# Optimization experiments

Hardware: AMD Instinct MI355X
Metric: run time of the kernel (lower is better)

Reference implementation:

```python
import jax, jax.numpy as jnp
import numpy as np

NUM_HEADS = 12
DIM_HEAD = 64
HIDDEN = 768


def _get_rel_pos(size, rel_pos):
    # q_size == k_size: relative coords in [0, 2*size-2]
    idx = jnp.arange(size)[:, None] - jnp.arange(size)[None, :] + (size - 1)
    return rel_pos[idx]  # (size, size, dim_head)


def setup_inputs() -> dict:
    key = jax.random.key(0)
    ks = jax.random.split(key, 5)
    B, H, W, C = 4, 32, 32, HIDDEN
    x = jax.random.normal(ks[0], (B, H, W, C), dtype=jnp.float32)
    w_qkv = jax.random.normal(ks[1], (C, 3 * NUM_HEADS * DIM_HEAD), dtype=jnp.float32) * (C ** -0.5)
    w_out = jax.random.normal(ks[2], (NUM_HEADS * DIM_HEAD, C), dtype=jnp.float32) * ((NUM_HEADS * DIM_HEAD) ** -0.5)
    b_out = jnp.zeros((C,), dtype=jnp.float32)
    rel_pos_h = jax.random.normal(ks[3], (2 * H - 1, DIM_HEAD), dtype=jnp.float32) * 0.02
    rel_pos_w = jax.random.normal(ks[4], (2 * W - 1, DIM_HEAD), dtype=jnp.float32) * 0.02
    return {"x": x, "w_qkv": w_qkv, "w_out": w_out, "b_out": b_out,
            "rel_pos_h": rel_pos_h, "rel_pos_w": rel_pos_w}


def reference(x, w_qkv, w_out, b_out, rel_pos_h, rel_pos_w):
    B, H, W, C = x.shape
    N = H * W
    nh, dh = NUM_HEADS, DIM_HEAD
    # qkv projection: (B, N, 3*nh*dh) split as (qkv, head, dim)
    qkv = x.reshape(B, N, C) @ w_qkv
    qkv = qkv.reshape(B, N, 3, nh, dh).transpose(2, 0, 3, 1, 4)  # (3, B, nh, N, dh)
    q, k, v = qkv[0], qkv[1], qkv[2]
    scale = dh ** -0.5
    attn = jnp.einsum('bhnd,bhmd->bhnm', q, k) * scale  # (B, nh, N, N)
    # decomposed relative positional bias (heads folded into batch)
    Rh = _get_rel_pos(H, rel_pos_h)  # (H, H, dh)
    Rw = _get_rel_pos(W, rel_pos_w)  # (W, W, dh)
    r_q = q.reshape(B * nh, H, W, dh)
    rel_h = jnp.einsum('bhwc,hkc->bhwk', r_q, Rh)  # (B*nh, H, W, H)
    rel_w = jnp.einsum('bhwc,wkc->bhwk', r_q, Rw)  # (B*nh, H, W, W)
    attn = (attn.reshape(B * nh, H, W, H, W)
            + rel_h[:, :, :, :, None]
            + rel_w[:, :, :, None, :]).reshape(B, nh, N, N)
    attn = jax.nn.softmax(attn, axis=-1)
    out = jnp.einsum('bhnm,bhmd->bhnd', attn, v)  # (B, nh, N, dh)
    out = out.transpose(0, 2, 1, 3).reshape(B, N, nh * dh)
    return out @ w_out + b_out  # (B, N, hidden)
```

## Files before the change

kernel.cpp:

```cpp
#include <hip/hip_runtime.h>
#include <cstdint>

#define DEV __device__ __forceinline__

typedef __bf16  bf16x8 __attribute__((ext_vector_type(8)));
typedef short   s16x8  __attribute__((ext_vector_type(8)));
typedef float   f32x4  __attribute__((ext_vector_type(4)));

#define QSCALE 0.18033688011112042f
#define MOFF   17.312340490667560f

DEV unsigned short f2bf(float f){
  union { float f; unsigned u; } v; v.f = f;
  unsigned r = v.u + 0x7fffu + ((v.u >> 16) & 1u);
  return (unsigned short)(r >> 16);
}

DEV unsigned pk2(float lo, float hi){
  unsigned a = __builtin_bit_cast(unsigned, lo) + 0x8000u;
  unsigned b = __builtin_bit_cast(unsigned, hi) + 0x8000u;
  return __builtin_amdgcn_perm(b, a, 0x07060302);
}

DEV void gl2lds16(const void* g, void* l){
  __builtin_amdgcn_global_load_lds((__attribute__((address_space(1))) void*)(void*)(g),
                                   (__attribute__((address_space(3))) void*)(l), 16, 0, 0);
}

DEV f32x4 mfma16(bf16x8 a, bf16x8 b, f32x4 c){
  return __builtin_amdgcn_mfma_f32_16x16x32_bf16(a, b, c, 0, 0, 0);
}

__global__ __launch_bounds__(256) void prep_kernel(const float* __restrict__ x,
                                                   short* __restrict__ xb,
                                                   const float* __restrict__ rph,
                                                   const float* __restrict__ rpw,
                                                   short* __restrict__ rphb,
                                                   short* __restrict__ rpwb,
                                                   const float* __restrict__ w_qkv,
                                                   short* __restrict__ wqT,
                                                   const float* __restrict__ w_out,
                                                   short* __restrict__ woT){
  __shared__ float tb[32][33];
  int b = blockIdx.x;
  if (b < 1536){
    int i = b * 256 + threadIdx.x;
    const float4* in4 = (const float4*)x;
    float4 f0 = in4[i*2], f1 = in4[i*2+1];
    s16x8 o;
    o[0]=(short)f2bf(f0.x); o[1]=(short)f2bf(f0.y); o[2]=(short)f2bf(f0.z); o[3]=(short)f2bf(f0.w);
    o[4]=(short)f2bf(f1.x); o[5]=(short)f2bf(f1.y); o[6]=(short)f2bf(f1.z); o[7]=(short)f2bf(f1.w);
    *(s16x8*)(xb + i*8) = o;
  } else if (b == 1536){
    int t = threadIdx.x;
    for (int j = 0; j < 16; j++){
      int idx = t*16 + j;
      if (idx < 4032){
        rphb[idx] = (short)f2bf(rph[idx] * 8.f);
        rpwb[idx] = (short)f2bf(rpw[idx] * 8.f);
      }
    }
  } else {
    const float* in; short* out; int R, C, bx, by;
    if (b < 3265){ int t = b - 1537; in = w_qkv; out = wqT; R = 768; C = 2304; bx = t % 72; by = t / 72; }
    else         { int t = b - 3265; in = w_out; out = woT; R = 768; C = 768;  bx = t % 24; by = t / 24; }
    int tx = threadIdx.x & 31, ty = threadIdx.x >> 5;
    int c0 = bx * 32, r0 = by * 32;
    for (int i = 0; i < 4; i++)
      tb[ty + i*8][tx] = in[(r0 + ty + i*8)*C + c0 + tx];
    __syncthreads();
    for (int i = 0; i < 4; i++)
      out[(c0 + ty + i*8)*R + r0 + tx] = (short)f2bf(tb[tx][ty + i*8]);
  }
}

__global__ __launch_bounds__(256) void qkv_gemm_kernel(const short* __restrict__ xb,
                                                       const short* __restrict__ wqT,
                                                       short* __restrict__ qb,
                                                       short* __restrict__ kb,
                                                       short* __restrict__ vb){
  __shared__ __align__(16) short As[128*64];
  __shared__ __align__(16) short Bs[96*64];
  const int tid = threadIdx.x, lane = tid & 63, wv = tid >> 6;
  const int quad = lane >> 4, mi = lane & 15;
  const int m0 = blockIdx.x * 128, n0 = blockIdx.y * 96;
  const int wrow = wv >> 1, wcol = wv & 1;
  const int srow = lane >> 3, scs = lane & 7;
  const int sc = scs ^ (srow & 7);
  f32x4 acc[4][3] = {};
  for (int k0 = 0; k0 < 768; k0 += 64){
    __syncthreads();
    for (int i = 0; i < 4; i++){
      int rbase = i*32 + wv*8;
      int row = rbase + srow;
      gl2lds16(xb + (m0+row)*768 + k0 + sc*8, As + rbase*64 + lane*8);
    }
    for (int i = 0; i < 3; i++){
      int rbase = i*32 + wv*8;
      int row = rbase + srow;
      gl2lds16(wqT + (n0+row)*768 + k0 + sc*8, Bs + rbase*64 + lane*8);
    }
    __syncthreads();
    bf16x8 a[2][4], b[2][3];
#pragma unroll
    for (int kk = 0; kk < 2; kk++){
      int ccs = ((quad + kk*4) ^ (mi & 7)) * 8;
      for (int mt = 0; mt < 4; mt++) a[kk][mt] = *(const bf16x8*)(As + (wrow*64 + mt*16 + mi)*64 + ccs);
      for (int nt = 0; nt < 3; nt++) b[kk][nt] = *(const bf16x8*)(Bs + (wcol*48 + nt*16 + mi)*64 + ccs);
    }
#pragma unroll
    for (int kk = 0; kk < 2; kk++)
      for (int mt = 0; mt < 4; mt++)
        for (int nt = 0; nt < 3; nt++)
          acc[mt][nt] = mfma16(a[kk][mt], b[kk][nt], acc[mt][nt]);
  }
  const int which = n0 / 768;
  const float qs = (which == 0) ? QSCALE : 1.0f;
  for (int nt = 0; nt < 3; nt++){
    int j = n0 + wcol*48 + nt*16 + mi;
    int rem = j % 768;
    int head = rem >> 6, d = rem & 63;
    short* dst = (which == 0) ? qb : (which == 1) ? kb : vb;
    for (int mt = 0; mt < 4; mt++)
      for (int r = 0; r < 4; r++){
        int m = m0 + wrow*64 + mt*16 + quad*4 + r;
        int bh = (m >> 10)*12 + head;
        dst[((bh << 10) + (m & 1023))*64 + d] = (short)f2bf(acc[mt][nt][r] * qs);
      }
  }
}

__global__ __launch_bounds__(256) void relvt_kernel(const short* __restrict__ qb,
                                                    const short* __restrict__ rphb,
                                                    const short* __restrict__ rpwb,
                                                    float* __restrict__ relHT,
                                                    float* __restrict__ relW,
                                                    const short* __restrict__ vb,
                                                    short* __restrict__ vtb){
  __shared__ __align__(16) short T[64*64];
  if (blockIdx.x < 1536){
    int wv = threadIdx.x >> 6, lane = threadIdx.x & 63;
    int bid = blockIdx.x*4 + wv;
    int quad = lane >> 4, mi = lane & 15;
    f32x4 acc[2] = {};
    if (bid < 3072){
      int bh = bid >> 6, rest = bid & 63, h = rest >> 1, half = rest & 1;
      const short* qr = qb + (bh*1024 + h*32 + half*16 + mi)*64;
      bf16x8 a0 = *(const bf16x8*)(qr + quad*8);
      bf16x8 a1 = *(const bf16x8*)(qr + 32 + quad*8);
      for (int nt = 0; nt < 2; nt++){
        int kh = nt*16 + mi;
        const short* rr = rphb + (h - kh + 31)*64;
        bf16x8 b0 = *(const bf16x8*)(rr + quad*8);
        bf16x8 b1 = *(const bf16x8*)(rr + 32 + quad*8);
        acc[nt] = mfma16(a0, b0, acc[nt]);
        acc[nt] = mfma16(a1, b1, acc[nt]);
      }
      for (int nt = 0; nt < 2; nt++){
        f32x4 o;
        for (int r = 0; r < 4; r++) o[r] = acc[nt][r] - MOFF;
        *(f32x4*)&relHT[bh*32768 + (nt*16 + mi)*1024 + h*32 + half*16 + quad*4] = o;
      }
    } else {
      int bid2 = bid - 3072, w = bid2 / 96, rt = bid2 % 96;
      int rg = rt*16 + mi, bh = rg >> 5, h = rg & 31;
      const short* qr = qb + (bh*1024 + h*32 + w)*64;
      bf16x8 a0 = *(const bf16x8*)(qr + quad*8);
      bf16x8 a1 = *(const bf16x8*)(qr + 32 + quad*8);
      for (int nt = 0; nt < 2; nt++){
        int kw = nt*16 + mi;
        const short* rr = rpwb + (w - kw + 31)*64;
        bf16x8 b0 = *(const bf16x8*)(rr + quad*8);
        bf16x8 b1 = *(const bf16x8*)(rr + 32 + quad*8);
        acc[nt] = mfma16(a0, b0, acc[nt]);
        acc[nt] = mfma16(a1, b1, acc[nt]);
      }
      for (int nt = 0; nt < 2; nt++)
        for (int r = 0; r < 4; r++){
          int rowg = rt*16 + quad*4 + r;
          relW[(rowg*32 + w)*32 + nt*16 + mi] = acc[nt][r];
        }
    }
  } else {
    int blk = blockIdx.x - 1536;
    int t = threadIdx.x;
    int bh = blk >> 4, t0 = (blk & 15) * 64;
    const short* src = vb + (bh*1024 + t0)*64;
    for (int p = 0; p < 2; p++){
      int row = p*32 + (t >> 3);
      int c = (t & 7) ^ (row & 7);
      gl2lds16(src + row*64 + c*8, T + p*2048 + t*8);
    }
    __syncthreads();
    int d = t >> 2, k4 = t & 3;
    short vals[16];
    for (int j = 0; j < 16; j++){
      int k = k4 + j*4;
      int cs = (d >> 3) ^ (k & 7);
      vals[j] = T[k*64 + cs*8 + (d & 7)];
    }
    short* dst = vtb + (bh*64 + d)*1024 + t0;
    for (int j = 0; j < 16; j++)
      dst[k4 + j*4] = vals[j];
  }
}

__global__ __launch_bounds__(256, 3) void flash_kernel(const short* __restrict__ qb,
                                                       const short* __restrict__ kb,
                                                       const short* __restrict__ vtb,
                                                       const float* __restrict__ relHT,
                                                       const float* __restrict__ relW,
                                                       short* __restrict__ ao){
  __shared__ __align__(16) short Qt[64*64];
  __shared__ __align__(16) short Kt[64*64];
  __shared__ __align__(16) short Vt[64*64];
  __shared__ __align__(16) short Pt[64*64];
  __shared__ __align__(16) float rHs[32*64];
  __shared__ __align__(16) float rWs[64*32];
  const int tid = threadIdx.x, lane = tid & 63, wv = tid >> 6;
  const int quad = lane >> 4, mi = lane & 15;
  const int bh = blockIdx.y, n0 = blockIdx.x * 64;
  const int sw0 = (quad ^ (mi & 7)) * 8;
  const int sw1 = ((quad + 4) ^ (mi & 7)) * 8;
  const int qrow = wv*16 + mi;
  const int srow = lane >> 3;

  const short* kg = kb  + bh*1024*64;
  const short* vg = vtb + bh*64*1024;

  {
    const short* qg  = qb    + (bh*1024 + n0)*64;
    const float* rhg = relHT + bh*32768 + n0;
    const float* rwg = relW  + (bh*1024 + n0)*32;
    for (int i = 0; i < 2; i++){
      int slab = wv*2 + i, rbase = slab*8;
      int row = rbase + srow;
      int c = (lane & 7) ^ (row & 7);
      gl2lds16(qg + row*64 + c*8, Qt + rbase*64 + lane*8);
      int khrow = i*16 + wv*4 + (lane >> 4);
      gl2lds16(rhg + khrow*1024 + (lane & 15)*4, rHs + i*1024 + wv*256 + lane*4);
      gl2lds16(rwg + slab*256 + lane*4, rWs + slab*256 + lane*4);
    }
  }
  __syncthreads();

  bf16x8 qf0 = *(const bf16x8*)(Qt + qrow*64 + sw0);
  bf16x8 qf1 = *(const bf16x8*)(Qt + qrow*64 + sw1);
  float rw[2][4];
#pragma unroll
  for (int s = 0; s < 2; s++)
    for (int r = 0; r < 4; r++)
      rw[s][r] = rWs[qrow*32 + s*16 + quad*4 + r];

  f32x4 O[4] = {};
  float l_ = 0.f;

  for (int step = 0; step < 16; step++){
    {
      const short* kt = kg + step*64*64;
      for (int i = 0; i < 2; i++){
        int slab = wv*2 + i, rbase = slab*8;
        int row = rbase + srow;
        int c = (lane & 7) ^ (row & 7);
        gl2lds16(kt + row*64 + c*8, Kt + rbase*64 + lane*8);
        gl2lds16(vg + row*1024 + step*64 + c*8, Vt + rbase*64 + lane*8);
      }
    }
    __syncthreads();

    f32x4 S[4];
#pragma unroll
    for (int nt = 0; nt < 4; nt++){
      bf16x8 kf0 = *(const bf16x8*)(Kt + (nt*16 + mi)*64 + sw0);
      bf16x8 kf1 = *(const bf16x8*)(Kt + (nt*16 + mi)*64 + sw1);
      f32x4 c = {};
      c = mfma16(kf0, qf0, c);
      c = mfma16(kf1, qf1, c);
      S[nt] = c;
    }
    float kh0 = rHs[(2*step)*64 + qrow];
    float kh1 = rHs[(2*step + 1)*64 + qrow];
#pragma unroll
    for (int nt = 0; nt < 4; nt++){
      float kh = (nt & 2) ? kh1 : kh0;
      for (int r = 0; r < 4; r++){
        float p = __builtin_amdgcn_exp2f(S[nt][r] + kh + rw[nt & 1][r]);
        S[nt][r] = p;
        l_ += p;
      }
    }
#pragma unroll
    for (int nt = 0; nt < 4; nt++){
      unsigned u0 = pk2(S[nt][0], S[nt][1]);
      unsigned u1 = pk2(S[nt][2], S[nt][3]);
      int chunk = (2*nt + (quad >> 1)) ^ (mi & 7);
      uint2 uu; uu.x = u0; uu.y = u1;
      *(uint2*)(Pt + qrow*64 + chunk*8 + (quad & 1)*4) = uu;
    }
    bf16x8 p0 = *(const bf16x8*)(Pt + qrow*64 + sw0);
    bf16x8 p1 = *(const bf16x8*)(Pt + qrow*64 + sw1);
#pragma unroll
    for (int t = 0; t < 4; t++){
      bf16x8 v0 = *(const bf16x8*)(Vt + (t*16 + mi)*64 + sw0);
      bf16x8 v1 = *(const bf16x8*)(Vt + (t*16 + mi)*64 + sw1);
      O[t] = mfma16(p0, v0, O[t]);
      O[t] = mfma16(p1, v1, O[t]);
    }
    __syncthreads();
  }

  l_ += __shfl_xor(l_, 16, 64);
  l_ += __shfl_xor(l_, 32, 64);
  float inv[4];
#pragma unroll
  for (int r = 0; r < 4; r++) inv[r] = 1.f / __shfl(l_, quad*4 + r, 64);
  int b_ = bh / 12, head = bh % 12;
#pragma unroll
  for (int t = 0; t < 4; t++)
    for (int r = 0; r < 4; r++){
      int n = n0 + wv*16 + quad*4 + r;
      ao[(b_*1024 + n)*768 + head*64 + t*16 + mi] = (short)f2bf(O[t][r] * inv[r]);
    }
}

__global__ __launch_bounds__(256) void proj_kernel(const short* __restrict__ ao,
                                                   const short* __restrict__ woT,
                                                   const float* __restrict__ bias,
                                                   float* __restrict__ out){
  __shared__ __align__(16) short As[64*64];
  __shared__ __align__(16) short Bs[96*64];
  const int tid = threadIdx.x, lane = tid & 63, wv = tid >> 6;
  const int quad = lane >> 4, mi = lane & 15;
  const int m0 = blockIdx.x * 64, n0 = blockIdx.y * 96;
  const int wrow = wv >> 1, wcol = wv & 1;
  const int srow = lane >> 3, sc = (lane & 7) ^ (srow & 7);
  f32x4 acc[2][3] = {};
  for (int k0 = 0; k0 < 768; k0 += 64){
    __syncthreads();
    for (int i = 0; i < 2; i++){
      int rbase = i*32 + wv*8, row = rbase + srow;
      gl2lds16(ao + (m0+row)*768 + k0 + sc*8, As + rbase*64 + lane*8);
    }
    for (int i = 0; i < 3; i++){
      int rbase = i*32 + wv*8, row = rbase + srow;
      gl2lds16(woT + (n0+row)*768 + k0 + sc*8, Bs + rbase*64 + lane*8);
    }
    __syncthreads();
    bf16x8 a[2][2], b[2][3];
#pragma unroll
    for (int kk = 0; kk < 2; kk++){
      int ccs = ((quad + kk*4) ^ (mi & 7)) * 8;
      for (int mt = 0; mt < 2; mt++) a[kk][mt] = *(const bf16x8*)(As + (wrow*32 + mt*16 + mi)*64 + ccs);
      for (int nt = 0; nt < 3; nt++) b[kk][nt] = *(const bf16x8*)(Bs + (wcol*48 + nt*16 + mi)*64 + ccs);
    }
#pragma unroll
    for (int kk = 0; kk < 2; kk++)
      for (int mt = 0; mt < 2; mt++)
        for (int nt = 0; nt < 3; nt++)
          acc[mt][nt] = mfma16(a[kk][mt], b[kk][nt], acc[mt][nt]);
  }
  for (int nt = 0; nt < 3; nt++){
    int j = n0 + wcol*48 + nt*16 + mi;
    float bj = bias[j];
    for (int mt = 0; mt < 2; mt++)
      for (int r = 0; r < 4; r++){
        int m = m0 + wrow*32 + mt*16 + quad*4 + r;
        out[m*768 + j] = acc[mt][nt][r] + bj;
      }
  }
}

extern "C" void kernel_launch(void* const* d_in, const int* in_sizes, int n_in,
                              void* d_out, int out_size, void* d_ws, size_t ws_size,
                              hipStream_t stream){
  const float* x     = (const float*)d_in[0];
  const float* w_qkv = (const float*)d_in[1];
  const float* w_out = (const float*)d_in[2];
  const float* b_out = (const float*)d_in[3];
  const float* rph   = (const float*)d_in[4];
  const float* rpw   = (const float*)d_in[5];
  float* out = (float*)d_out;
  char* ws = (char*)d_ws;
  short* xb    = (short*)(ws + 0);
  short* wqT   = (short*)(ws + 6291456);
  short* woT   = (short*)(ws + 9830400);
  short* qb    = (short*)(ws + 11010048);
  short* kb    = (short*)(ws + 17301504);
  short* vb    = (short*)(ws + 23592960);
  short* vtb   = (short*)(ws + 29884416);
  float* relHT = (float*)(ws + 36175872);
  float* relW  = (float*)(ws + 42467328);
  short* rphb  = (short*)(ws + 48758784);
  short* rpwb  = (short*)(ws + 48775168);
  short* ao    = xb;

  prep_kernel<<<3841, 256, 0, stream>>>(x, xb, rph, rpw, rphb, rpwb, w_qkv, wqT, w_out, woT);
  qkv_gemm_kernel<<<dim3(32, 24), 256, 0, stream>>>(xb, wqT, qb, kb, vb);
  relvt_kernel<<<2304, 256, 0, stream>>>(qb, rphb, rpwb, relHT, relW, vb, vtb);
  flash_kernel<<<dim3(16, 48), 256, 0, stream>>>(qb, kb, vtb, relHT, relW, ao);
  proj_kernel<<<dim3(64, 8), 256, 0, stream>>>(ao, woT, b_out, out);
}
```

Measured before the change: 155.9 us.

## Fuse V transpose into QKV GEMM and compute rel_h bias inside flash kernel

After: 153.8 us. About the same (-1.4%).

```diff
diff --git a/kernel.cpp b/kernel.cpp
--- a/kernel.cpp
+++ b/kernel.cpp
@@ -78,7 +78,7 @@
                                                        const short* __restrict__ wqT,
                                                        short* __restrict__ qb,
                                                        short* __restrict__ kb,
-                                                       short* __restrict__ vb){
+                                                       short* __restrict__ vtb){
   __shared__ __align__(16) short As[128*64];
   __shared__ __align__(16) short Bs[96*64];
   const int tid = threadIdx.x, lane = tid & 63, wv = tid >> 6;
@@ -115,101 +115,67 @@
           acc[mt][nt] = mfma16(a[kk][mt], b[kk][nt], acc[mt][nt]);
   }
   const int which = n0 / 768;
-  const float qs = (which == 0) ? QSCALE : 1.0f;
-  for (int nt = 0; nt < 3; nt++){
-    int j = n0 + wcol*48 + nt*16 + mi;
-    int rem = j % 768;
-    int head = rem >> 6, d = rem & 63;
-    short* dst = (which == 0) ? qb : (which == 1) ? kb : vb;
-    for (int mt = 0; mt < 4; mt++)
-      for (int r = 0; r < 4; r++){
-        int m = m0 + wrow*64 + mt*16 + quad*4 + r;
-        int bh = (m >> 10)*12 + head;
-        dst[((bh << 10) + (m & 1023))*64 + d] = (short)f2bf(acc[mt][nt][r] * qs);
-      }
-  }
-}
-
-__global__ __launch_bounds__(256) void relvt_kernel(const short* __restrict__ qb,
-                                                    const short* __restrict__ rphb,
-                                                    const short* __restrict__ rpwb,
-                                                    float* __restrict__ relHT,
-                                                    float* __restrict__ relW,
-                                                    const short* __restrict__ vb,
-                                                    short* __restrict__ vtb){
-  __shared__ __align__(16) short T[64*64];
-  if (blockIdx.x < 1536){
-    int wv = threadIdx.x >> 6, lane = threadIdx.x & 63;
-    int bid = blockIdx.x*4 + wv;
-    int quad = lane >> 4, mi = lane & 15;
-    f32x4 acc[2] = {};
-    if (bid < 3072){
-      int bh = bid >> 6, rest = bid & 63, h = rest >> 1, half = rest & 1;
-      const short* qr = qb + (bh*1024 + h*32 + half*16 + mi)*64;
-      bf16x8 a0 = *(const bf16x8*)(qr + quad*8);
-      bf16x8 a1 = *(const bf16x8*)(qr + 32 + quad*8);
-      for (int nt = 0; nt < 2; nt++){
-        int kh = nt*16 + mi;
-        const short* rr = rphb + (h - kh + 31)*64;
-        bf16x8 b0 = *(const bf16x8*)(rr + quad*8);
-        bf16x8 b1 = *(const bf16x8*)(rr + 32 + quad*8);
-        acc[nt] = mfma16(a0, b0, acc[nt]);
-        acc[nt] = mfma16(a1, b1, acc[nt]);
-      }
-      for (int nt = 0; nt < 2; nt++){
-        f32x4 o;
-        for (int r = 0; r < 4; r++) o[r] = acc[nt][r] - MOFF;
-        *(f32x4*)&relHT[bh*32768 + (nt*16 + mi)*1024 + h*32 + half*16 + quad*4] = o;
-      }
-    } else {
-      int bid2 = bid - 3072, w = bid2 / 96, rt = bid2 % 96;
-      int rg = rt*16 + mi, bh = rg >> 5, h = rg & 31;
-      const short* qr = qb + (bh*1024 + h*32 + w)*64;
-      bf16x8 a0 = *(const bf16x8*)(qr + quad*8);
-      bf16x8 a1 = *(const bf16x8*)(qr + 32 + quad*8);
-      for (int nt = 0; nt < 2; nt++){
-        int kw = nt*16 + mi;
-        const short* rr = rpwb + (w - kw + 31)*64;
-        bf16x8 b0 = *(const bf16x8*)(rr + quad*8);
-        bf16x8 b1 = *(const bf16x8*)(rr + 32 + quad*8);
-        acc[nt] = mfma16(a0, b0, acc[nt]);
-        acc[nt] = mfma16(a1, b1, acc[nt]);
-      }
-      for (int nt = 0; nt < 2; nt++)
+  if (which == 2){
+    for (int nt = 0; nt < 3; nt++){
+      int j = n0 + wcol*48 + nt*16 + mi;
+      int rem = j % 768;
+      int head = rem >> 6, d = rem & 63;
+      for (int mt = 0; mt < 4; mt++)
         for (int r = 0; r < 4; r++){
-          int rowg = rt*16 + quad*4 + r;
-          relW[(rowg*32 + w)*32 + nt*16 + mi] = acc[nt][r];
+          int m = m0 + wrow*64 + mt*16 + quad*4 + r;
+          int bh = (m >> 10)*12 + head;
+          vtb[((bh*64 + d) << 10) + (m & 1023)] = (short)f2bf(acc[mt][nt][r]);
         }
     }
   } else {
-    int blk = blockIdx.x - 1536;
-    int t = threadIdx.x;
-    int bh = blk >> 4, t0 = (blk & 15) * 64;
-    const short* src = vb + (bh*1024 + t0)*64;
-    for (int p = 0; p < 2; p++){
-      int row = p*32 + (t >> 3);
-      int c = (t & 7) ^ (row & 7);
-      gl2lds16(src + row*64 + c*8, T + p*2048 + t*8);
-    }
-    __syncthreads();
-    int d = t >> 2, k4 = t & 3;
-    short vals[16];
-    for (int j = 0; j < 16; j++){
-      int k = k4 + j*4;
-      int cs = (d >> 3) ^ (k & 7);
-      vals[j] = T[k*64 + cs*8 + (d & 7)];
-    }
-    short* dst = vtb + (bh*64 + d)*1024 + t0;
-    for (int j = 0; j < 16; j++)
-      dst[k4 + j*4] = vals[j];
-  }
+    const float qs = (which == 0) ? QSCALE : 1.0f;
+    short* dst = (which == 0) ? qb : kb;
+    for (int nt = 0; nt < 3; nt++){
+      int j = n0 + wcol*48 + nt*16 + mi;
+      int rem = j % 768;
+      int head = rem >> 6, d = rem & 63;
+      for (int mt = 0; mt < 4; mt++)
+        for (int r = 0; r < 4; r++){
+          int m = m0 + wrow*64 + mt*16 + quad*4 + r;
+          int bh = (m >> 10)*12 + head;
+          dst[((bh << 10) + (m & 1023))*64 + d] = (short)f2bf(acc[mt][nt][r] * qs);
+        }
+    }
+  }
+}
+
+__global__ __launch_bounds__(256) void relw_kernel(const short* __restrict__ qb,
+                                                   const short* __restrict__ rpwb,
+                                                   float* __restrict__ relW){
+  int wv = threadIdx.x >> 6, lane = threadIdx.x & 63;
+  int bid2 = blockIdx.x*4 + wv;
+  int quad = lane >> 4, mi = lane & 15;
+  f32x4 acc[2] = {};
+  int w = bid2 / 96, rt = bid2 % 96;
+  int rg = rt*16 + mi, bh = rg >> 5, h = rg & 31;
+  const short* qr = qb + (bh*1024 + h*32 + w)*64;
+  bf16x8 a0 = *(const bf16x8*)(qr + quad*8);
+  bf16x8 a1 = *(const bf16x8*)(qr + 32 + quad*8);
+  for (int nt = 0; nt < 2; nt++){
+    int kw = nt*16 + mi;
+    const short* rr = rpwb + (w - kw + 31)*64;
+    bf16x8 b0 = *(const bf16x8*)(rr + quad*8);
+    bf16x8 b1 = *(const bf16x8*)(rr + 32 + quad*8);
+    acc[nt] = mfma16(a0, b0, acc[nt]);
+    acc[nt] = mfma16(a1, b1, acc[nt]);
+  }
+  for (int nt = 0; nt < 2; nt++)
+    for (int r = 0; r < 4; r++){
+      int rowg = rt*16 + quad*4 + r;
+      relW[(rowg*32 + w)*32 + nt*16 + mi] = acc[nt][r];
+    }
 }
 
 __global__ __launch_bounds__(256, 3) void flash_kernel(const short* __restrict__ qb,
                                                        const short* __restrict__ kb,
                                                        const short* __restrict__ vtb,
-                                                       const float* __restrict__ relHT,
                                                        const float* __restrict__ relW,
+                                                       const short* __restrict__ rphb,
                                                        short* __restrict__ ao){
   __shared__ __align__(16) short Qt[64*64];
   __shared__ __align__(16) short Kt[64*64];
@@ -229,16 +195,13 @@
   const short* vg = vtb + bh*64*1024;
 
   {
-    const short* qg  = qb    + (bh*1024 + n0)*64;
-    const float* rhg = relHT + bh*32768 + n0;
-    const float* rwg = relW  + (bh*1024 + n0)*32;
+    const short* qg  = qb   + (bh*1024 + n0)*64;
+    const float* rwg = relW + (bh*1024 + n0)*32;
     for (int i = 0; i < 2; i++){
       int slab = wv*2 + i, rbase = slab*8;
       int row = rbase + srow;
       int c = (lane & 7) ^ (row & 7);
       gl2lds16(qg + row*64 + c*8, Qt + rbase*64 + lane*8);
-      int khrow = i*16 + wv*4 + (lane >> 4);
-      gl2lds16(rhg + khrow*1024 + (lane & 15)*4, rHs + i*1024 + wv*256 + lane*4);
       gl2lds16(rwg + slab*256 + lane*4, rWs + slab*256 + lane*4);
     }
   }
@@ -251,6 +214,22 @@
   for (int s = 0; s < 2; s++)
     for (int r = 0; r < 4; r++)
       rw[s][r] = rWs[qrow*32 + s*16 + quad*4 + r];
+
+  {
+    int h = (n0 + wv*16) >> 5;
+    const short* rp = rphb + (h + 31 - mi)*64;
+#pragma unroll
+    for (int khb = 0; khb < 2; khb++){
+      const short* rk = rp - khb*1024;
+      bf16x8 a0 = *(const bf16x8*)(rk + quad*8);
+      bf16x8 a1 = *(const bf16x8*)(rk + 32 + quad*8);
+      f32x4 c = {};
+      c = mfma16(a0, qf0, c);
+      c = mfma16(a1, qf1, c);
+      for (int r = 0; r < 4; r++)
+        rHs[(khb*16 + quad*4 + r)*64 + wv*16 + mi] = c[r] - MOFF;
+    }
+  }
 
   f32x4 O[4] = {};
   float l_ = 0.f;
@@ -386,17 +365,15 @@
   short* woT   = (short*)(ws + 9830400);
   short* qb    = (short*)(ws + 11010048);
   short* kb    = (short*)(ws + 17301504);
-  short* vb    = (short*)(ws + 23592960);
   short* vtb   = (short*)(ws + 29884416);
-  float* relHT = (float*)(ws + 36175872);
   float* relW  = (float*)(ws + 42467328);
   short* rphb  = (short*)(ws + 48758784);
   short* rpwb  = (short*)(ws + 48775168);
   short* ao    = xb;
 
   prep_kernel<<<3841, 256, 0, stream>>>(x, xb, rph, rpw, rphb, rpwb, w_qkv, wqT, w_out, woT);
-  qkv_gemm_kernel<<<dim3(32, 24), 256, 0, stream>>>(xb, wqT, qb, kb, vb);
-  relvt_kernel<<<2304, 256, 0, stream>>>(qb, rphb, rpwb, relHT, relW, vb, vtb);
-  flash_kernel<<<dim3(16, 48), 256, 0, stream>>>(qb, kb, vtb, relHT, relW, ao);
+  qkv_gemm_kernel<<<dim3(32, 24), 256, 0, stream>>>(xb, wqT, qb, kb, vtb);
+  relw_kernel<<<768, 256, 0, stream>>>(qb, rpwb, relW);
+  flash_kernel<<<dim3(16, 48), 256, 0, stream>>>(qb, kb, vtb, relW, rphb, ao);
   proj_kernel<<<dim3(64, 8), 256, 0, stream>>>(ao, woT, b_out, out);
 }
```
